# Performance work log

Hardware: AMD Instinct MI355X
Metric: run time of the kernel (lower is better)

## Reference

```python
import jax, jax.numpy as jnp
import numpy as np

C = 80           # foreground classes
B, N = 8, 4000   # images, proposals per image
K_PRE = 2048     # pre-NMS candidates per image (fixed-shape stand-in for torch.where filtering)
DET = 100        # detection_per_image
SCORE_THRESH = 0.01
NMS_THRESH = 0.5
MIN_AREA = 0.1
BBOX_W = (10.0, 10.0, 5.0, 5.0)
CLIP = float(np.log(1000.0 / 16.0))
CLS_OFFSET = 4096.0               # > max image coordinate, for batched (per-class) NMS


def setup_inputs() -> dict:
    key = jax.random.key(0)
    k1, k2, k3, k4 = jax.random.split(key, 4)
    p1 = jax.random.uniform(k1, (B, N, 2)) * 800.0
    wh = jax.random.uniform(k2, (B, N, 2)) * 200.0 + 1.0
    proposals = jnp.concatenate([p1, p1 + wh], axis=-1)          # [B,N,4] x1,y1,x2,y2
    label_pre = jax.random.normal(k3, (B, N, C + 1), dtype=jnp.float32)
    bbox_pre = jax.random.normal(k4, (B, N, (C + 1) * 4), dtype=jnp.float32) * 0.5
    return {"label_pre": label_pre, "bbox_pre": bbox_pre, "proposals": proposals}


def decode_boxes(deltas, props):
    w = props[..., 2] - props[..., 0]
    h = props[..., 3] - props[..., 1]
    cx = props[..., 0] + 0.5 * w
    cy = props[..., 1] + 0.5 * h
    dx = deltas[..., 0] / BBOX_W[0]
    dy = deltas[..., 1] / BBOX_W[1]
    dw = jnp.minimum(deltas[..., 2] / BBOX_W[2], CLIP)
    dh = jnp.minimum(deltas[..., 3] / BBOX_W[3], CLIP)
    pcx = dx * w + cx
    pcy = dy * h + cy
    pw = jnp.exp(dw) * w
    ph = jnp.exp(dh) * h
    return jnp.stack([pcx - 0.5 * pw, pcy - 0.5 * ph,
                      pcx + 0.5 * pw, pcy + 0.5 * ph], axis=-1)


def pairwise_iou(b):
    # b [K,4] -> [K,K]
    area = jnp.maximum(b[:, 2] - b[:, 0], 0.0) * jnp.maximum(b[:, 3] - b[:, 1], 0.0)
    lt = jnp.maximum(b[:, None, :2], b[None, :, :2])
    rb = jnp.minimum(b[:, None, 2:], b[None, :, 2:])
    wh = jnp.maximum(rb - lt, 0.0)
    inter = wh[..., 0] * wh[..., 1]
    union = area[:, None] + area[None, :] - inter
    return inter / jnp.maximum(union, 1e-9)


def greedy_nms_keep(boxes, valid):
    # boxes already sorted by score (descending); returns kept mask
    K = boxes.shape[0]
    iou = pairwise_iou(boxes)
    idx = jnp.arange(K)

    def body(i, keep):
        sup = (iou[i] > NMS_THRESH) & (idx > i) & keep[i]
        return keep & ~sup

    return jax.lax.fori_loop(0, K, body, valid)


def process_image(logits, deltas, props):
    probs = jax.nn.softmax(logits, axis=-1)            # [N, C+1]
    scores = probs[:, 1:].reshape(-1)                  # [N*C]
    d = deltas[:, 4:].reshape(N, C, 4)                 # drop background deltas
    boxes = decode_boxes(d, props[:, None, :]).reshape(-1, 4)   # [N*C, 4]
    labels = jnp.broadcast_to(jnp.arange(1, C + 1), (N, C)).reshape(-1)
    area = (boxes[:, 3] - boxes[:, 1]) * (boxes[:, 2] - boxes[:, 0])
    valid = (scores > SCORE_THRESH) & (area > MIN_AREA)
    masked = jnp.where(valid, scores, -1.0)
    top_scores, top_idx = jax.lax.top_k(masked, K_PRE)
    top_boxes = boxes[top_idx]
    top_labels = labels[top_idx]
    keep0 = top_scores > 0.0
    # batched_nms: per-class coordinate offset so classes never suppress each other
    off = (top_labels.astype(top_boxes.dtype) * CLS_OFFSET)[:, None]
    keep = greedy_nms_keep(top_boxes + off, keep0)
    final = jnp.where(keep, top_scores, -1.0)
    det_scores, det_idx = jax.lax.top_k(final, DET)
    return top_boxes[det_idx], det_scores, top_labels[det_idx]


def reference(label_pre, bbox_pre, proposals):
    # returns (boxes [B,DET,4], scores [B,DET], labels [B,DET]); entries with score<0 are padding
    return jax.vmap(process_image)(label_pre, bbox_pre, proposals)
```

## Files before the change

kernel.cpp:

```cpp
#include <hip/hip_runtime.h>
#include <stdint.h>

#define B_ 8
#define N_ 4000
#define C_ 80
#define NC_ (N_ * C_)
#define KP_ 2048
#define CAND_ 4096
#define SLOTS_ 32
#define SLOTCAP_ 128
#define DET_ 100
#define NW_ 32
#define CLIP_ 4.135166556742356f

#define PB_ 16
#define IB_ (N_ / PB_)
#define CB_ 64
#define FB_ 128
#define NBLK_ ((NC_ / 4 + 255) / 256)

typedef unsigned long long u64;

__device__ __forceinline__ void decode4(const float4 pr, const float4 d,
                                        float& x1, float& y1, float& x2, float& y2) {
  float w = pr.z - pr.x, h = pr.w - pr.y;
  float cx = pr.x + 0.5f * w, cy = pr.y + 0.5f * h;
  float dx = d.x / 10.0f, dy = d.y / 10.0f;
  float dw = fminf(d.z / 5.0f, CLIP_), dh = fminf(d.w / 5.0f, CLIP_);
  float pcx = dx * w + cx, pcy = dy * h + cy;
  float pw = expf(dw) * w, ph = expf(dh) * h;
  x1 = pcx - 0.5f * pw; y1 = pcy - 0.5f * ph;
  x2 = pcx + 0.5f * pw; y2 = pcy + 0.5f * ph;
}

__device__ __forceinline__ u64 shflx64(u64 x, int m) {
  unsigned lo = (unsigned)__shfl_xor((int)(unsigned)x, m, 64);
  unsigned hi = (unsigned)__shfl_xor((int)(unsigned)(x >> 32), m, 64);
  return ((u64)hi << 32) | lo;
}

__global__ __launch_bounds__(256) void k_scores(const float* __restrict__ logits,
                                                uint32_t* __restrict__ keys,
                                                uint32_t* __restrict__ imgHist) {
  __shared__ float lds[PB_ * 81];
  __shared__ float mArr[PB_], dArr[PB_];
  __shared__ uint32_t hcnt[CB_];
  int blk = blockIdx.x;
  int b = blk / IB_, lb = blk - b * IB_;
  int p0 = b * N_ + lb * PB_;
  int t = threadIdx.x;
  if (t < CB_) hcnt[t] = 0;
  const float4* src = (const float4*)(logits + (size_t)p0 * 81);
  for (int k = t; k < PB_ * 81 / 4; k += 256) ((float4*)lds)[k] = src[k];
  __syncthreads();
  if (t < PB_) {
    const float* lp = lds + t * 81;
    float m = lp[0];
    for (int i = 1; i <= C_; ++i) m = fmaxf(m, lp[i]);
    float denom = 0.f;
    for (int i = 0; i <= C_; ++i) denom += expf(lp[i] - m);
    mArr[t] = m; dArr[t] = denom;
  }
  __syncthreads();
#pragma unroll
  for (int iter = 0; iter < PB_ * C_ / 256; ++iter) {
    int e = iter * 256 + t;
    int pp = e / C_, c = e - pp * C_;
    float lv = lds[pp * 81 + c + 1];
    float score = expf(lv - mArr[pp]) / dArr[pp];
    uint32_t key = 0;
    if (score > 0.01f) {
      key = __float_as_uint(score);
      atomicAdd(&hcnt[(key >> 20) - 960], 1u);
    }
    keys[(size_t)p0 * C_ + e] = key;
  }
  __syncthreads();
  if (t < CB_ && hcnt[t]) atomicAdd(&imgHist[b * CB_ + t], hcnt[t]);
}

__global__ __launch_bounds__(256) void k_refine(const uint32_t* __restrict__ keys,
                                                const uint32_t* __restrict__ imgHist,
                                                uint32_t* __restrict__ fineHist) {
  __shared__ int s_cb;
  int blk = blockIdx.x;
  int b = blk / NBLK_, lb = blk - b * NBLK_;
  int t = threadIdx.x;
  if (t < 64) {
    uint32_t v = imgHist[b * CB_ + t];
#pragma unroll
    for (int d = 1; d < 64; d <<= 1) {
      uint32_t o = __shfl_down(v, d);
      v += (t + d < 64) ? o : 0;
    }
    uint32_t nxt = __shfl_down(v, 1);
    if (t == 63) nxt = 0;
    uint32_t total = __shfl(v, 0);
    if (t == 0 && total < KP_) s_cb = -1;
    if (total >= KP_ && v >= KP_ && nxt < KP_) s_cb = t;
  }
  __syncthreads();
  int cb = s_cb;
  if (cb < 0) return;
  int ti = lb * 256 + t;
  if (ti >= NC_ / 4) return;
  uint4 k4 = ((const uint4*)(keys + (size_t)b * NC_))[ti];
  uint32_t want = (uint32_t)(cb + 960);
  uint32_t kv[4] = {k4.x, k4.y, k4.z, k4.w};
#pragma unroll
  for (int q = 0; q < 4; ++q)
    if ((kv[q] >> 20) == want)
      atomicAdd(&fineHist[b * FB_ + ((kv[q] >> 13) & (FB_ - 1))], 1u);
}

__global__ __launch_bounds__(256) void k_compact(const uint32_t* __restrict__ keys,
                                                 const uint32_t* __restrict__ imgHist,
                                                 const uint32_t* __restrict__ fineHist,
                                                 uint32_t* __restrict__ cnt,
                                                 u64* __restrict__ cand) {
  __shared__ int s_cb;
  __shared__ uint32_t s_tail;
  __shared__ uint32_t s_thr;
  int blk = blockIdx.x;
  int b = blk / NBLK_, lb = blk - b * NBLK_;
  int t = threadIdx.x;
  if (t < 64) {
    uint32_t v = imgHist[b * CB_ + t];
#pragma unroll
    for (int d = 1; d < 64; d <<= 1) {
      uint32_t o = __shfl_down(v, d);
      v += (t + d < 64) ? o : 0;
    }
    uint32_t nxt = __shfl_down(v, 1);
    if (t == 63) nxt = 0;
    uint32_t total = __shfl(v, 0);
    if (t == 0 && total < KP_) { s_cb = -1; s_tail = 0; }
    if (total >= KP_ && v >= KP_ && nxt < KP_) { s_cb = t; s_tail = nxt; }
  }
  __syncthreads();
  int cb = s_cb;
  if (cb < 0) {
    if (t == 0) s_thr = 1u;
  } else if (t < 64) {
    uint32_t f0 = fineHist[b * FB_ + 2 * t];
    uint32_t f1 = fineHist[b * FB_ + 2 * t + 1];
    uint32_t v = f0 + f1;
#pragma unroll
    for (int d = 1; d < 64; d <<= 1) {
      uint32_t o = __shfl_down(v, d);
      v += (t + d < 64) ? o : 0;
    }
    uint32_t nxt = __shfl_down(v, 1);
    if (t == 63) nxt = 0;
    uint32_t tail = s_tail;
    bool c0 = (tail + v >= KP_);
    bool c1 = (tail + nxt + f1 >= KP_);
    bool cN = (tail + nxt >= KP_);
    if (c0 && !c1) s_thr = ((uint32_t)(cb + 960) << 20) | ((uint32_t)(2 * t) << 13);
    if (c1 && !cN) s_thr = ((uint32_t)(cb + 960) << 20) | ((uint32_t)(2 * t + 1) << 13);
  }
  __syncthreads();
  uint32_t thrb = s_thr;
  int ti = lb * 256 + t;
  if (ti >= NC_ / 4) return;
  uint4 k4 = ((const uint4*)(keys + (size_t)b * NC_))[ti];
  int slot = (ti >> 4) & (SLOTS_ - 1);
  uint32_t kv[4] = {k4.x, k4.y, k4.z, k4.w};
  int ns = 0;
#pragma unroll
  for (int q = 0; q < 4; ++q) ns += (kv[q] >= thrb) ? 1 : 0;
  if (ns == 0) return;
  uint32_t pos = atomicAdd(&cnt[(b * SLOTS_ + slot) * 16], (uint32_t)ns);
  u64* seg = cand + (size_t)b * CAND_ + slot * SLOTCAP_;
  uint32_t baseIdx = (uint32_t)(ti * 4);
#pragma unroll
  for (int q = 0; q < 4; ++q) {
    if (kv[q] >= thrb) {
      if (pos < SLOTCAP_)
        seg[pos] = ((u64)kv[q] << 32) | (uint32_t)(~(baseIdx + q));
      ++pos;
    }
  }
}

__global__ __launch_bounds__(1024) void k_sort_topk(
    const u64* __restrict__ cand,
    const float* __restrict__ bbox, const float* __restrict__ props,
    float* __restrict__ topScore, int* __restrict__ topLabel,
    float* __restrict__ topBox, float* __restrict__ nmsBox) {
  __shared__ u64 sh[CAND_];
  int b = blockIdx.x, t = threadIdx.x;
  u64 v[4];
  const u64* cb2 = cand + (size_t)b * CAND_;
#pragma unroll
  for (int e = 0; e < 4; ++e) v[e] = cb2[4 * t + e];

  auto cmpsw = [](u64& a, u64& b2, bool desc) {
    bool sw = desc ? (a < b2) : (a > b2);
    if (sw) { u64 tmp = a; a = b2; b2 = tmp; }
  };

  for (unsigned size = 2; size <= CAND_; size <<= 1) {
    unsigned s = size >> 1;
    if (s >= 256) {
#pragma unroll
      for (int e = 0; e < 4; ++e) sh[4 * t + e] = v[e];
      __syncthreads();
      for (; s >= 256; s >>= 1) {
        for (unsigned i = t; i < CAND_; i += 1024) {
          unsigned j = i ^ s;
          if (j > i) {
            bool desc = ((i & size) == 0);
            u64 a = sh[i], b3 = sh[j];
            bool sw = desc ? (a < b3) : (a > b3);
            if (sw) { sh[i] = b3; sh[j] = a; }
          }
        }
        __syncthreads();
      }
#pragma unroll
      for (int e = 0; e < 4; ++e) v[e] = sh[4 * t + e];
    }
    for (; s >= 4; s >>= 1) {
      int lm = (int)(s >> 2);
      bool lower = ((t & lm) == 0);
      bool desc = ((((unsigned)(4 * t)) & size) == 0);
      bool takeMax = (lower == desc);
#pragma unroll
      for (int e = 0; e < 4; ++e) {
        u64 p = shflx64(v[e], lm);
        v[e] = takeMax ? (v[e] > p ? v[e] : p) : (v[e] < p ? v[e] : p);
      }
    }
    if (s == 2) {
      bool desc = ((((unsigned)(4 * t)) & size) == 0);
      cmpsw(v[0], v[2], desc);
      cmpsw(v[1], v[3], desc);
      s >>= 1;
    }
    if (s == 1) {
      bool d0 = ((((unsigned)(4 * t)) & size) == 0);
      bool d1 = ((((unsigned)(4 * t + 2)) & size) == 0);
      cmpsw(v[0], v[1], d0);
      cmpsw(v[2], v[3], d1);
    }
  }
  if (t < KP_ / 4) {
    float sc[4];
    int lb4[4];
    float4 bx[4], nb[4];
#pragma unroll
    for (int e = 0; e < 4; ++e) {
      u64 key = v[e];
      if (key == 0ull) {
        sc[e] = -1.0f; lb4[e] = 0;
        bx[e] = make_float4(0.f, 0.f, 0.f, 0.f);
        nb[e] = make_float4(0.f, 0.f, 0.f, 0.f);
      } else {
        uint32_t sbits = (uint32_t)(key >> 32);
        uint32_t idx = ~((uint32_t)key);
        int n = idx / C_, c = idx % C_;
        float4 pr4 = ((const float4*)props)[(size_t)b * N_ + n];
        float4 d = ((const float4*)(bbox + ((size_t)b * N_ + n) * ((C_ + 1) * 4)))[c + 1];
        float x1, y1, x2, y2;
        decode4(pr4, d, x1, y1, x2, y2);
        float off = (float)(c + 1) * 4096.0f;
        sc[e] = __uint_as_float(sbits);
        lb4[e] = c + 1;
        bx[e] = make_float4(x1, y1, x2, y2);
        nb[e] = make_float4(x1 + off, y1 + off, x2 + off, y2 + off);
      }
    }
    size_t o = (size_t)b * KP_ + 4 * t;
    *(float4*)&topScore[o] = make_float4(sc[0], sc[1], sc[2], sc[3]);
    *(int4*)&topLabel[o] = make_int4(lb4[0], lb4[1], lb4[2], lb4[3]);
    float4* tbp = (float4*)(topBox + o * 4);
    float4* nbp = (float4*)(nmsBox + o * 4);
#pragma unroll
    for (int e = 0; e < 4; ++e) { tbp[e] = bx[e]; nbp[e] = nb[e]; }
  }
}

__global__ __launch_bounds__(64) void k_supmat(const float* __restrict__ nmsBox,
                                               u64* __restrict__ sup) {
  int blk = blockIdx.x;
  int b = blk / 528, r = blk - b * 528;
  int ti = 0, rem = r;
  while (rem >= 32 - ti) { rem -= 32 - ti; ++ti; }
  int tj = ti + rem;
  __shared__ float4 shj[64];
  __shared__ float sha[64];
  int l = threadIdx.x;
  const float4* boxes = (const float4*)(nmsBox + (size_t)b * KP_ * 4);
  float4 bj0 = boxes[tj * 64 + l];
  shj[l] = bj0;
  sha[l] = fmaxf(bj0.z - bj0.x, 0.f) * fmaxf(bj0.w - bj0.y, 0.f);
  int i = ti * 64 + l;
  float4 bi = boxes[i];
  float areai = fmaxf(bi.z - bi.x, 0.f) * fmaxf(bi.w - bi.y, 0.f);
  __syncthreads();
  u64 bits = 0;
  for (int jj = 0; jj < 64; ++jj) {
    int j = tj * 64 + jj;
    if (j > i) {
      float4 bj = shj[jj];
      float ltx = fmaxf(bi.x, bj.x), lty = fmaxf(bi.y, bj.y);
      float rbx = fminf(bi.z, bj.z), rby = fminf(bi.w, bj.w);
      float iw = fmaxf(rbx - ltx, 0.f), ih = fmaxf(rby - lty, 0.f);
      float inter = iw * ih;
      float uni = areai + sha[jj] - inter;
      float iou = inter / fmaxf(uni, 1e-9f);
      if (iou > 0.5f) bits |= (1ull << jj);
    }
  }
  sup[((size_t)b * KP_ + i) * NW_ + tj] = bits;
}

__global__ __launch_bounds__(64) void k_nms_scan(const u64* __restrict__ sup,
                                                 const float* __restrict__ topScore,
                                                 const int* __restrict__ topLabel,
                                                 const float* __restrict__ topBox,
                                                 float* __restrict__ out) {
  int b = blockIdx.x, l = threadIdx.x;
  int h = l >> 5, w = l & 31;
  const u64* base = sup + (size_t)b * KP_ * NW_;
  const float* ts = topScore + (size_t)b * KP_;
  const int* tl = topLabel + (size_t)b * KP_;
  const float4* tb = (const float4*)(topBox + (size_t)b * KP_ * 4);
  unsigned m32 = 0;
#pragma unroll
  for (int j = 0; j < 8; ++j) {
    float4 s4 = ((const float4*)ts)[l * 8 + j];
    if (!(s4.x > 0.f)) m32 |= 1u << (4 * j + 0);
    if (!(s4.y > 0.f)) m32 |= 1u << (4 * j + 1);
    if (!(s4.z > 0.f)) m32 |= 1u << (4 * j + 2);
    if (!(s4.w > 0.f)) m32 |= 1u << (4 * j + 3);
  }
  u64 removed = ((u64)__shfl(m32, 2 * w + 1) << 32) | (u64)__shfl(m32, 2 * w);

  int outCount = 0;
  auto emitRow = [&](int row, bool kept) {
    if (l == (outCount & 63)) {
      float4 bx = tb[row];
      out[((size_t)b * DET_ + outCount) * 4 + 0] = bx.x;
      out[((size_t)b * DET_ + outCount) * 4 + 1] = bx.y;
      out[((size_t)b * DET_ + outCount) * 4 + 2] = bx.z;
      out[((size_t)b * DET_ + outCount) * 4 + 3] = bx.w;
      out[B_ * DET_ * 4 + (size_t)b * DET_ + outCount] = kept ? ts[row] : -1.0f;
      out[B_ * DET_ * 4 + B_ * DET_ + (size_t)b * DET_ + outCount] = (float)tl[row];
    }
    ++outCount;
  };

  u64 ra[32], rb[32];
  auto loadc = [&](u64* dst, int c) {
    const u64* p = base + ((size_t)c * 64 + h * 32) * NW_ + w;
#pragma unroll
    for (int k = 0; k < 32; ++k) dst[k] = p[(size_t)k * NW_];
  };
  auto chunk = [&](u64* cur, int c) -> bool {
    u64 rm = __shfl(removed, c);
    unsigned rml = (unsigned)rm, rmh = (unsigned)(rm >> 32);
#pragma unroll
    for (int k = 0; k < 32; ++k) {
      unsigned dlo = __builtin_amdgcn_readlane((unsigned)cur[k], c);
      unsigned dhi = __builtin_amdgcn_readlane((unsigned)(cur[k] >> 32), c);
      if (!((rml >> k) & 1u)) { rml |= dlo; rmh |= dhi; }
    }
#pragma unroll
    for (int k = 0; k < 32; ++k) {
      unsigned dlo = __builtin_amdgcn_readlane((unsigned)cur[k], 32 + c);
      unsigned dhi = __builtin_amdgcn_readlane((unsigned)(cur[k] >> 32), 32 + c);
      if (!((rmh >> k) & 1u)) { rml |= dlo; rmh |= dhi; }
    }
    u64 rmfull = ((u64)rmh << 32) | rml;
    u64 kb = ~rmfull;
    while (kb) {
      if (outCount >= DET_) return true;
      int k = __builtin_ctzll(kb);
      kb &= kb - 1;
      emitRow(c * 64 + k, true);
    }
    if (outCount >= DET_) return true;
    unsigned kmask = h ? ~rmh : ~rml;
    u64 acc = 0;
#pragma unroll
    for (int k = 0; k < 32; ++k)
      acc |= ((kmask >> k) & 1u) ? cur[k] : 0ull;
    acc |= __shfl_xor(acc, 32);
    removed = (l == c) ? rmfull : removed;
    if (l < 32 && l >= c) removed |= acc;
    return false;
  };

  bool done = false;
  loadc(ra, 0);
  for (int c = 0; c < NW_ && !done; c += 2) {
    if (c + 1 < NW_) loadc(rb, c + 1);
    done = chunk(ra, c);
    if (!done) {
      if (c + 2 < NW_) loadc(ra, c + 2);
      done = chunk(rb, c + 1);
    }
  }
  if (outCount < DET_) {
    for (int c2 = 0; c2 < NW_ && outCount < DET_; ++c2) {
      u64 rm = __shfl(removed, c2);
      while (rm && outCount < DET_) {
        int k = __builtin_ctzll(rm);
        rm &= rm - 1;
        emitRow(c2 * 64 + k, false);
      }
    }
  }
}

extern "C" void kernel_launch(void* const* d_in, const int* in_sizes, int n_in,
                              void* d_out, int out_size, void* d_ws, size_t ws_size,
                              hipStream_t stream) {
  const float* label_pre = (const float*)d_in[0];
  const float* bbox_pre = (const float*)d_in[1];
  const float* props = (const float*)d_in[2];
  float* out = (float*)d_out;

  char* ws = (char*)d_ws;
  size_t off = 0;
  auto alloc = [&](size_t bytes) -> void* {
    void* p = ws + off;
    off = (off + bytes + 255) & ~(size_t)255;
    return p;
  };

  uint32_t* keys = (uint32_t*)alloc((size_t)B_ * NC_ * 4);
  size_t zero_begin = off;
  uint32_t* imgHist = (uint32_t*)alloc((size_t)B_ * CB_ * 4);
  uint32_t* fineHist = (uint32_t*)alloc((size_t)B_ * FB_ * 4);
  uint32_t* cnt = (uint32_t*)alloc((size_t)B_ * SLOTS_ * 16 * 4);
  u64* cand = (u64*)alloc((size_t)B_ * CAND_ * 8);
  size_t zero_end = off;
  float* topScore = (float*)alloc((size_t)B_ * KP_ * 4);
  int* topLabel = (int*)alloc((size_t)B_ * KP_ * 4);
  float* topBox = (float*)alloc((size_t)B_ * KP_ * 16);
  float* nmsBox = (float*)alloc((size_t)B_ * KP_ * 16);
  u64* sup = (u64*)alloc((size_t)B_ * KP_ * NW_ * 8);

  if (off > ws_size) return;

  hipMemsetAsync(ws + zero_begin, 0, zero_end - zero_begin, stream);

  k_scores<<<B_ * IB_, 256, 0, stream>>>(label_pre, keys, imgHist);
  k_refine<<<B_ * NBLK_, 256, 0, stream>>>(keys, imgHist, fineHist);
  k_compact<<<B_ * NBLK_, 256, 0, stream>>>(keys, imgHist, fineHist, cnt, cand);
  k_sort_topk<<<B_, 1024, 0, stream>>>(cand, bbox_pre, props,
                                       topScore, topLabel, topBox, nmsBox);
  k_supmat<<<B_ * 528, 64, 0, stream>>>(nmsBox, sup);
  k_nms_scan<<<B_, 64, 0, stream>>>(sup, topScore, topLabel, topBox, out);
}
```

Baseline: 212.5 us.

## Replace single-block bitonic sort with parallel rank-by-counting top-K scatter

The per-image bitonic sort of 4096 candidates, which ran in one 1024-thread block per image, is replaced by a rank kernel spread over 16 blocks per image. Each thread counts how many candidate keys exceed its own key, then writes its decoded box straight to that rank slot if the rank is below K_PRE. Output buffers are now zeroed by the memset, because slots left empty would otherwise hold stale data. This uses far more blocks across the GPU, at the cost of O(n^2) comparisons read from LDS and a larger memset.

```diff
diff --git a/kernel.cpp b/kernel.cpp
--- a/kernel.cpp
+++ b/kernel.cpp
@@ -19,6 +19,9 @@
 #define FB_ 128
 #define NBLK_ ((NC_ / 4 + 255) / 256)
 
+#define RT_ 256
+#define RBLK_ (CAND_ / RT_)
+
 typedef unsigned long long u64;
 
 __device__ __forceinline__ void decode4(const float4 pr, const float4 d,
@@ -33,12 +36,6 @@
   x2 = pcx + 0.5f * pw; y2 = pcy + 0.5f * ph;
 }
 
-__device__ __forceinline__ u64 shflx64(u64 x, int m) {
-  unsigned lo = (unsigned)__shfl_xor((int)(unsigned)x, m, 64);
-  unsigned hi = (unsigned)__shfl_xor((int)(unsigned)(x >> 32), m, 64);
-  return ((u64)hi << 32) | lo;
-}
-
 __global__ __launch_bounds__(256) void k_scores(const float* __restrict__ logits,
                                                 uint32_t* __restrict__ keys,
                                                 uint32_t* __restrict__ imgHist) {
@@ -183,101 +180,42 @@
   }
 }
 
-__global__ __launch_bounds__(1024) void k_sort_topk(
+__global__ __launch_bounds__(256) void k_rank_topk(
     const u64* __restrict__ cand,
     const float* __restrict__ bbox, const float* __restrict__ props,
     float* __restrict__ topScore, int* __restrict__ topLabel,
     float* __restrict__ topBox, float* __restrict__ nmsBox) {
   __shared__ u64 sh[CAND_];
-  int b = blockIdx.x, t = threadIdx.x;
-  u64 v[4];
+  int blk = blockIdx.x;
+  int b = blk / RBLK_, lb = blk - b * RBLK_;
+  int t = threadIdx.x;
   const u64* cb2 = cand + (size_t)b * CAND_;
-#pragma unroll
-  for (int e = 0; e < 4; ++e) v[e] = cb2[4 * t + e];
-
-  auto cmpsw = [](u64& a, u64& b2, bool desc) {
-    bool sw = desc ? (a < b2) : (a > b2);
-    if (sw) { u64 tmp = a; a = b2; b2 = tmp; }
-  };
-
-  for (unsigned size = 2; size <= CAND_; size <<= 1) {
-    unsigned s = size >> 1;
-    if (s >= 256) {
-#pragma unroll
-      for (int e = 0; e < 4; ++e) sh[4 * t + e] = v[e];
-      __syncthreads();
-      for (; s >= 256; s >>= 1) {
-        for (unsigned i = t; i < CAND_; i += 1024) {
-          unsigned j = i ^ s;
-          if (j > i) {
-            bool desc = ((i & size) == 0);
-            u64 a = sh[i], b3 = sh[j];
-            bool sw = desc ? (a < b3) : (a > b3);
-            if (sw) { sh[i] = b3; sh[j] = a; }
-          }
-        }
-        __syncthreads();
-      }
-#pragma unroll
-      for (int e = 0; e < 4; ++e) v[e] = sh[4 * t + e];
-    }
-    for (; s >= 4; s >>= 1) {
-      int lm = (int)(s >> 2);
-      bool lower = ((t & lm) == 0);
-      bool desc = ((((unsigned)(4 * t)) & size) == 0);
-      bool takeMax = (lower == desc);
-#pragma unroll
-      for (int e = 0; e < 4; ++e) {
-        u64 p = shflx64(v[e], lm);
-        v[e] = takeMax ? (v[e] > p ? v[e] : p) : (v[e] < p ? v[e] : p);
-      }
-    }
-    if (s == 2) {
-      bool desc = ((((unsigned)(4 * t)) & size) == 0);
-      cmpsw(v[0], v[2], desc);
-      cmpsw(v[1], v[3], desc);
-      s >>= 1;
-    }
-    if (s == 1) {
-      bool d0 = ((((unsigned)(4 * t)) & size) == 0);
-      bool d1 = ((((unsigned)(4 * t + 2)) & size) == 0);
-      cmpsw(v[0], v[1], d0);
-      cmpsw(v[2], v[3], d1);
-    }
-  }
-  if (t < KP_ / 4) {
-    float sc[4];
-    int lb4[4];
-    float4 bx[4], nb[4];
-#pragma unroll
-    for (int e = 0; e < 4; ++e) {
-      u64 key = v[e];
-      if (key == 0ull) {
-        sc[e] = -1.0f; lb4[e] = 0;
-        bx[e] = make_float4(0.f, 0.f, 0.f, 0.f);
-        nb[e] = make_float4(0.f, 0.f, 0.f, 0.f);
-      } else {
-        uint32_t sbits = (uint32_t)(key >> 32);
-        uint32_t idx = ~((uint32_t)key);
-        int n = idx / C_, c = idx % C_;
-        float4 pr4 = ((const float4*)props)[(size_t)b * N_ + n];
-        float4 d = ((const float4*)(bbox + ((size_t)b * N_ + n) * ((C_ + 1) * 4)))[c + 1];
-        float x1, y1, x2, y2;
-        decode4(pr4, d, x1, y1, x2, y2);
-        float off = (float)(c + 1) * 4096.0f;
-        sc[e] = __uint_as_float(sbits);
-        lb4[e] = c + 1;
-        bx[e] = make_float4(x1, y1, x2, y2);
-        nb[e] = make_float4(x1 + off, y1 + off, x2 + off, y2 + off);
-      }
-    }
-    size_t o = (size_t)b * KP_ + 4 * t;
-    *(float4*)&topScore[o] = make_float4(sc[0], sc[1], sc[2], sc[3]);
-    *(int4*)&topLabel[o] = make_int4(lb4[0], lb4[1], lb4[2], lb4[3]);
-    float4* tbp = (float4*)(topBox + o * 4);
-    float4* nbp = (float4*)(nmsBox + o * 4);
-#pragma unroll
-    for (int e = 0; e < 4; ++e) { tbp[e] = bx[e]; nbp[e] = nb[e]; }
+  for (int k = t; k < CAND_ / 2; k += RT_)
+    ((ulonglong2*)sh)[k] = ((const ulonglong2*)cb2)[k];
+  u64 ki = cb2[lb * RT_ + t];
+  __syncthreads();
+  int cnt = 0;
+#pragma unroll 8
+  for (int j = 0; j < CAND_; j += 2) {
+    u64 a = sh[j];
+    u64 c2 = sh[j + 1];
+    cnt += (a > ki) ? 1 : 0;
+    cnt += (c2 > ki) ? 1 : 0;
+  }
+  if (ki != 0ull && cnt < KP_) {
+    uint32_t sbits = (uint32_t)(ki >> 32);
+    uint32_t idx = ~((uint32_t)ki);
+    int n = idx / C_, c = idx % C_;
+    float4 pr4 = ((const float4*)props)[(size_t)b * N_ + n];
+    float4 d = ((const float4*)(bbox + ((size_t)b * N_ + n) * ((C_ + 1) * 4)))[c + 1];
+    float x1, y1, x2, y2;
+    decode4(pr4, d, x1, y1, x2, y2);
+    float off = (float)(c + 1) * 4096.0f;
+    size_t o = (size_t)b * KP_ + (size_t)cnt;
+    topScore[o] = __uint_as_float(sbits);
+    topLabel[o] = c + 1;
+    ((float4*)topBox)[o] = make_float4(x1, y1, x2, y2);
+    ((float4*)nmsBox)[o] = make_float4(x1 + off, y1 + off, x2 + off, y2 + off);
   }
 }
 
@@ -437,11 +375,11 @@
   uint32_t* fineHist = (uint32_t*)alloc((size_t)B_ * FB_ * 4);
   uint32_t* cnt = (uint32_t*)alloc((size_t)B_ * SLOTS_ * 16 * 4);
   u64* cand = (u64*)alloc((size_t)B_ * CAND_ * 8);
-  size_t zero_end = off;
   float* topScore = (float*)alloc((size_t)B_ * KP_ * 4);
   int* topLabel = (int*)alloc((size_t)B_ * KP_ * 4);
   float* topBox = (float*)alloc((size_t)B_ * KP_ * 16);
   float* nmsBox = (float*)alloc((size_t)B_ * KP_ * 16);
+  size_t zero_end = off;
   u64* sup = (u64*)alloc((size_t)B_ * KP_ * NW_ * 8);
 
   if (off > ws_size) return;
@@ -451,8 +389,8 @@
   k_scores<<<B_ * IB_, 256, 0, stream>>>(label_pre, keys, imgHist);
   k_refine<<<B_ * NBLK_, 256, 0, stream>>>(keys, imgHist, fineHist);
   k_compact<<<B_ * NBLK_, 256, 0, stream>>>(keys, imgHist, fineHist, cnt, cand);
-  k_sort_topk<<<B_, 1024, 0, stream>>>(cand, bbox_pre, props,
-                                       topScore, topLabel, topBox, nmsBox);
+  k_rank_topk<<<B_ * RBLK_, RT_, 0, stream>>>(cand, bbox_pre, props,
+                                              topScore, topLabel, topBox, nmsBox);
   k_supmat<<<B_ * 528, 64, 0, stream>>>(nmsBox, sup);
   k_nms_scan<<<B_, 64, 0, stream>>>(sup, topScore, topLabel, topBox, out);
 }
```

Measured after the change: 221.0 us. +4.0%, slower.
